# Performance work log

Measured on AMD Instinct MI355X. Metric: run time of the kernel, lower is better.

## Reference

```python
import jax, jax.numpy as jnp
import numpy as np

LN_EPS = 1e-5


def _expert(x, w1, b1, gamma, beta, w2, b2):
    # Linear(input_dim,24) -> LayerNorm(24) -> SiLU -> (Dropout=id in eval) -> Linear(24,16) -> SiLU
    h = x @ w1 + b1                                  # [B,24]
    mu = jnp.mean(h, axis=-1, keepdims=True)
    var = jnp.mean(jnp.square(h - mu), axis=-1, keepdims=True)
    h = (h - mu) * jax.lax.rsqrt(var + LN_EPS) * gamma + beta
    h = jax.nn.silu(h)
    return jax.nn.silu(h @ w2 + b2)                  # [B,16]


def setup_inputs() -> dict:
    key = jax.random.key(0)
    ks = jax.random.split(key, 16)
    D = 16  # input_dim
    s = 0.1
    inp = {
        "x": jax.random.normal(ks[0], (2097152, D), dtype=jnp.float32),
        # gate: Linear(D,8) -> Tanh -> Linear(8,2)
        "gw1": jax.random.normal(ks[1], (D, 8), dtype=jnp.float32) * s,
        "gb1": jnp.zeros((8,), jnp.float32),
        "gw2": jax.random.normal(ks[2], (8, 2), dtype=jnp.float32) * s,
        "gb2": jnp.zeros((2,), jnp.float32),
        # expert1
        "e1w1": jax.random.normal(ks[3], (D, 24), dtype=jnp.float32) * s,
        "e1b1": jnp.zeros((24,), jnp.float32),
        "e1g": jnp.ones((24,), jnp.float32),
        "e1bn": jnp.zeros((24,), jnp.float32),
        "e1w2": jax.random.normal(ks[4], (24, 16), dtype=jnp.float32) * s,
        "e1b2": jnp.zeros((16,), jnp.float32),
        # expert2
        "e2w1": jax.random.normal(ks[5], (D, 24), dtype=jnp.float32) * s,
        "e2b1": jnp.zeros((24,), jnp.float32),
        "e2g": jnp.ones((24,), jnp.float32),
        "e2bn": jnp.zeros((24,), jnp.float32),
        "e2w2": jax.random.normal(ks[6], (24, 16), dtype=jnp.float32) * s,
        "e2b2": jnp.zeros((16,), jnp.float32),
        # trunk: Linear(16,16) -> SiLU -> (Dropout=id)
        "tw": jax.random.normal(ks[7], (16, 16), dtype=jnp.float32) * s,
        "tb": jnp.zeros((16,), jnp.float32),
        # heads
        "sw": jax.random.normal(ks[8], (16, 1), dtype=jnp.float32) * s,
        "sb": jnp.zeros((1,), jnp.float32),
        "hw": jax.random.normal(ks[9], (16, 2), dtype=jnp.float32) * s,
        "hb": jnp.zeros((2,), jnp.float32),
    }
    return inp


def reference(x, gw1, gb1, gw2, gb2,
              e1w1, e1b1, e1g, e1bn, e1w2, e1b2,
              e2w1, e2b1, e2g, e2bn, e2w2, e2b2,
              tw, tb, sw, sb, hw, hb):
    gate_logits = jnp.tanh(x @ gw1 + gb1) @ gw2 + gb2        # [B,2]
    gate_w = jax.nn.softmax(gate_logits, axis=-1)
    h1 = _expert(x, e1w1, e1b1, e1g, e1bn, e1w2, e1b2)       # [B,16]
    h2 = _expert(x, e2w1, e2b1, e2g, e2bn, e2w2, e2b2)       # [B,16]
    h = gate_w[:, :1] * h1 + gate_w[:, 1:] * h2              # [B,16]
    h = jax.nn.silu(h @ tw + tb)                             # trunk (dropout=id)
    strain = h @ sw + sb                                     # [B,1]
    hs = h @ hw + hb                                         # [B,2]
    tensile_raw = hs[:, :1]
    gap = jax.nn.softplus(hs[:, 1:])
    yield_strength = tensile_raw - gap
    return jnp.concatenate([strain, tensile_raw, yield_strength], axis=-1)  # [B,3]
```

## Files before the change

kernel.cpp:

```cpp
#include <hip/hip_runtime.h>

#define LN_EPS 1e-5f

typedef _Float16 f16x4 __attribute__((ext_vector_type(4)));
typedef float f32x4 __attribute__((ext_vector_type(4)));
typedef unsigned int u32;
typedef u32 u32x2 __attribute__((ext_vector_type(2)));

#if defined(__HIP_DEVICE_COMPILE__)
#  if __has_builtin(__builtin_amdgcn_mfma_f32_16x16x16f16)
#    define MFMA16(a, b, c) __builtin_amdgcn_mfma_f32_16x16x16f16(a, b, c, 0, 0, 0)
#  elif __has_builtin(__builtin_amdgcn_mfma_f32_16x16x16_f16)
#    define MFMA16(a, b, c) __builtin_amdgcn_mfma_f32_16x16x16_f16(a, b, c, 0, 0, 0)
#  else
#    error "no 16x16x16 f16 mfma builtin on device"
#  endif
#else
#  define MFMA16(a, b, c) (c)
#endif

__device__ __forceinline__ float fast_rcp(float x) { return __builtin_amdgcn_rcpf(x); }

__device__ __forceinline__ u32 pk2(float a, float b) {
    return __builtin_bit_cast(u32, __builtin_amdgcn_cvt_pkrtz(a, b));
}
__device__ __forceinline__ f16x4 mk4(float a, float b, float c, float d) {
    u32x2 t = {pk2(a, b), pk2(c, d)};
    return __builtin_bit_cast(f16x4, t);
}

__device__ __forceinline__ float silu_f(float a) {
    return a * fast_rcp(1.0f + __expf(-a));
}
__device__ __forceinline__ float tanh_f(float x) {
    return fmaf(2.0f, fast_rcp(1.0f + __expf(-2.0f * x)), -1.0f);
}
__device__ __forceinline__ float softplus_f(float x) {
    float e = __expf(-fabsf(x));
    return fmaxf(x, 0.0f) + __logf(1.0f + e);
}


__device__ __forceinline__ float aval(int m, int row, int k,
                                      const float* gw1, const float* gw2,
                                      const float* e1w1, const float* e1w2,
                                      const float* e2w1, const float* e2w2,
                                      const float* tw, const float* sw, const float* hw) {
    switch (m) {
        case 0:  return (row < 8) ? gw1[k * 8 + row] : 0.0f;
        case 1:  return ((row & 3) < 2 && k < 8) ? gw2[k * 2 + (row & 3)] : 0.0f;
        case 2:  return e1w1[k * 24 + row];
        case 3: {
            if (row < 8) return e1w1[k * 24 + 16 + row];
            if (row == 8) {
                float t = 0.0f;
                for (int j = 0; j < 24; ++j) t += e1w1[k * 24 + j];
                return t * (1.0f / 24.0f);
            }
            return 0.0f;
        }
        case 4:  return e1w2[k * 16 + row];
        case 5:  return (k < 8) ? e1w2[(16 + k) * 16 + row] : 0.0f;
        case 6:  return e2w1[k * 24 + row];
        case 7: {
            if (row < 8) return e2w1[k * 24 + 16 + row];
            if (row == 8) {
                float t = 0.0f;
                for (int j = 0; j < 24; ++j) t += e2w1[k * 24 + j];
                return t * (1.0f / 24.0f);
            }
            return 0.0f;
        }
        case 8:  return e2w2[k * 16 + row];
        case 9:  return (k < 8) ? e2w2[(16 + k) * 16 + row] : 0.0f;
        case 10: return tw[k * 16 + row];
        default:
            if (row == 0) return sw[k];
            if (row == 1) return hw[2 * k + 0];
            if (row == 2) return hw[2 * k + 1];
            return 0.0f;
    }
}

__device__ __forceinline__ float bval(int bf, int row,
                                      const float* gb1, const float* gb2,
                                      const float* e1b1, const float* e1b2,
                                      const float* e2b1, const float* e2b2,
                                      const float* tb, const float* sb, const float* hb) {
    switch (bf) {
        case 0:  return (row < 8) ? gb1[row] : 0.0f;
        case 1:  return ((row & 3) < 2) ? gb2[row & 3] : 0.0f;
        case 2:  return e1b1[row];
        case 3: {
            if (row < 8) return e1b1[16 + row];
            if (row == 8) {
                float t = 0.0f;
                for (int j = 0; j < 24; ++j) t += e1b1[j];
                return t * (1.0f / 24.0f);
            }
            return 0.0f;
        }
        case 4:  return e1b2[row];
        case 5:  return e2b1[row];
        case 6: {
            if (row < 8) return e2b1[16 + row];
            if (row == 8) {
                float t = 0.0f;
                for (int j = 0; j < 24; ++j) t += e2b1[j];
                return t * (1.0f / 24.0f);
            }
            return 0.0f;
        }
        case 7:  return e2b2[row];
        case 8:  return tb[row];
        default:
            if (row == 0) return sb[0];
            if (row == 1) return hb[0];
            if (row == 2) return hb[1];
            return 0.0f;
    }
}

__global__ void pack_frags(const float* __restrict__ gw1, const float* __restrict__ gb1,
                           const float* __restrict__ gw2, const float* __restrict__ gb2,
                           const float* __restrict__ e1w1, const float* __restrict__ e1b1,
                           const float* __restrict__ e1g, const float* __restrict__ e1bn,
                           const float* __restrict__ e1w2, const float* __restrict__ e1b2,
                           const float* __restrict__ e2w1, const float* __restrict__ e2b1,
                           const float* __restrict__ e2g, const float* __restrict__ e2bn,
                           const float* __restrict__ e2w2, const float* __restrict__ e2b2,
                           const float* __restrict__ tw, const float* __restrict__ tb,
                           const float* __restrict__ sw, const float* __restrict__ sb,
                           const float* __restrict__ hw, const float* __restrict__ hb,
                           u32* __restrict__ ws) {
    int t = blockIdx.x * blockDim.x + threadIdx.x;
    if (t < 1536) {
        int m = t >> 7, rem = t & 127, lane = rem >> 1, d = rem & 1;
        int row = lane & 15, k0 = (lane >> 4) * 4 + 2 * d;
        float v0 = aval(m, row, k0,     gw1, gw2, e1w1, e1w2, e2w1, e2w2, tw, sw, hw);
        float v1 = aval(m, row, k0 + 1, gw1, gw2, e1w1, e1w2, e2w1, e2w2, tw, sw, hw);
        ws[t] = pk2(v0, v1);
    } else if (t < 4096) {
        int f = t - 1536;
        int bf = f >> 8, rem = f & 255, lane = rem >> 2, r = rem & 3;
        int row = (lane >> 4) * 4 + r;
        float v = bval(bf, row, gb1, gb2, e1b1, e1b2, e2b1, e2b2, tb, sb, hb);
        ((float*)ws)[t] = v;
    } else if (t < 6144) {
        int f = t - 4096;
        int nf = f >> 8, rem = f & 255, lane = rem >> 2, r = rem & 3;
        int e = nf >> 2, w = nf & 3, g_ = lane >> 4;
        const float* ge = e ? e2g : e1g;
        const float* bne = e ? e2bn : e1bn;
        float v;
        if (w < 2) {
            int feat = g_ * 4 + r;
            v = (w == 0) ? ge[feat] : bne[feat];
        } else {
            int feat = 16 + g_ * 4 + r;
            v = (g_ < 2) ? ((w == 2) ? ge[feat] : bne[feat]) : 0.0f;
        }
        ((float*)ws)[t] = v;
    }
}

__global__ __launch_bounds__(256) void moe_mfma_kernel(const float* __restrict__ x,
                                                       const u32* __restrict__ ws,
                                                       float* __restrict__ out, int nrows) {
    __shared__ u32 lds[6144];
    for (int i = threadIdx.x; i < 6144; i += 256) lds[i] = ws[i];
    __syncthreads();

    int lane = threadIdx.x & 63;
    int g = lane >> 4, s = lane & 15;
    float mask0 = (g == 2) ? 0.0f : 1.0f;
    int wid = (blockIdx.x * blockDim.x + threadIdx.x) >> 6;
    int nw = (gridDim.x * blockDim.x) >> 6;

    auto LA  = [&](int m)  -> f16x4 { return *(const f16x4*)&lds[m * 128 + lane * 2]; };
    auto LB  = [&](int bf) -> f32x4 { return *(const f32x4*)&lds[1536 + bf * 256 + lane * 4]; };
    auto LNF = [&](int nf) -> f32x4 { return *(const f32x4*)&lds[4096 + nf * 256 + lane * 4]; };

    auto expert2 = [&](bool FIRST, int mA1a, int mA1b, int mA2a, int mA2b,
                       int bf1a, int bf1b, int bf2, int nf,
                       f16x4 Bx0, f16x4 Bx1, float sc0, float sc1,
                       f32x4& h0, f32x4& h1) {
        f16x4 A1a = LA(mA1a), A1b = LA(mA1b);
        f32x4 b1a = LB(bf1a), b1b = LB(bf1b);
        f32x4 C1_0 = MFMA16(A1a, Bx0, b1a);
        f32x4 C1_1 = MFMA16(A1a, Bx1, b1a);
        f32x4 C2_0 = MFMA16(A1b, Bx0, b1b);
        f32x4 C2_1 = MFMA16(A1b, Bx1, b1b);

        float mu0 = __shfl(C2_0[0], 32 + s, 64);
        float mu1 = __shfl(C2_1[0], 32 + s, 64);

        float E20 = 0.0f, E21 = 0.0f;
#pragma unroll
        for (int i = 0; i < 4; ++i) {
            E20 = fmaf(C1_0[i], C1_0[i], E20);
            E21 = fmaf(C1_1[i], C1_1[i], E21);
        }
        E20 = fmaf(C2_0[0] * mask0, C2_0[0], E20);
        E21 = fmaf(C2_1[0] * mask0, C2_1[0], E21);
#pragma unroll
        for (int i = 1; i < 4; ++i) {
            E20 = fmaf(C2_0[i], C2_0[i], E20);
            E21 = fmaf(C2_1[i], C2_1[i], E21);
        }
        E20 += __shfl_xor(E20, 16); E20 += __shfl_xor(E20, 32);
        E21 += __shfl_xor(E21, 16); E21 += __shfl_xor(E21, 32);
        float rstd0 = rsqrtf(fmaf(E20, 1.0f / 24.0f, -mu0 * mu0) + LN_EPS);
        float rstd1 = rsqrtf(fmaf(E21, 1.0f / 24.0f, -mu1 * mu1) + LN_EPS);

        f32x4 gc1 = LNF(nf + 0), bc1 = LNF(nf + 1), gc2 = LNF(nf + 2), bc2 = LNF(nf + 3);
        float sv0[8], sv1[8];
#pragma unroll
        for (int i = 0; i < 4; ++i) {
            sv0[i]     = silu_f(fmaf((C1_0[i] - mu0) * rstd0, gc1[i], bc1[i]));
            sv1[i]     = silu_f(fmaf((C1_1[i] - mu1) * rstd1, gc1[i], bc1[i]));
            sv0[4 + i] = silu_f(fmaf((C2_0[i] - mu0) * rstd0, gc2[i], bc2[i]));
            sv1[4 + i] = silu_f(fmaf((C2_1[i] - mu1) * rstd1, gc2[i], bc2[i]));
        }
        f16x4 B1_0 = mk4(sv0[0], sv0[1], sv0[2], sv0[3]);
        f16x4 B2_0 = mk4(sv0[4], sv0[5], sv0[6], sv0[7]);
        f16x4 B1_1 = mk4(sv1[0], sv1[1], sv1[2], sv1[3]);
        f16x4 B2_1 = mk4(sv1[4], sv1[5], sv1[6], sv1[7]);

        f16x4 A2a = LA(mA2a), A2b = LA(mA2b);
        f32x4 b2 = LB(bf2);
        f32x4 O0 = MFMA16(A2a, B1_0, b2);
        f32x4 O1 = MFMA16(A2a, B1_1, b2);
        O0 = MFMA16(A2b, B2_0, O0);
        O1 = MFMA16(A2b, B2_1, O1);

#pragma unroll
        for (int i = 0; i < 4; ++i) {
            float p0 = silu_f(O0[i]);
            float p1 = silu_f(O1[i]);
            if (FIRST) {
                h0[i] = sc0 * p0;
                h1[i] = sc1 * p1;
            } else {
                h0[i] = fmaf(sc0, p0, h0[i]);
                h1[i] = fmaf(sc1, p1, h1[i]);
            }
        }
    };

    int ntiles = (nrows + 15) >> 4;
    int nclamp = nrows - 1;

    auto loadx = [&](int tile) -> f32x4 {
        int r = tile * 16 + s;
        int rc = r < nrows ? r : nclamp;
        return *(const f32x4*)(x + (size_t)rc * 16 + g * 4);
    };

    int p0 = 2 * wid;
    f32x4 xv0, xv1;
    if (p0 < ntiles) {
        xv0 = loadx(p0);
        xv1 = loadx(p0 + 1 < ntiles ? p0 + 1 : p0);
    }

    for (int tp = p0; tp < ntiles; tp += 2 * nw) {
        int tnp = tp + 2 * nw;
        f32x4 xn0, xn1;
        {
            int t0n = tnp < ntiles ? tnp : tp;
            int t1n = tnp + 1 < ntiles ? tnp + 1 : t0n;
            xn0 = loadx(t0n);
            xn1 = loadx(t1n);
        }

        int r0 = tp * 16 + s;
        int r1 = (tp + 1) * 16 + s;
        f16x4 Bx0 = mk4(xv0[0], xv0[1], xv0[2], xv0[3]);
        f16x4 Bx1 = mk4(xv1[0], xv1[1], xv1[2], xv1[3]);

        f32x4 Cg0 = MFMA16(LA(0), Bx0, LB(0));
        f32x4 Cg1 = MFMA16(LA(0), Bx1, LB(0));
        f16x4 Bt0 = mk4(tanh_f(Cg0[0]), tanh_f(Cg0[1]), tanh_f(Cg0[2]), tanh_f(Cg0[3]));
        f16x4 Bt1 = mk4(tanh_f(Cg1[0]), tanh_f(Cg1[1]), tanh_f(Cg1[2]), tanh_f(Cg1[3]));
        f32x4 Cl0 = MFMA16(LA(1), Bt0, LB(1));
        f32x4 Cl1 = MFMA16(LA(1), Bt1, LB(1));
        float w00 = fast_rcp(1.0f + __expf(Cl0[1] - Cl0[0]));
        float w01 = 1.0f - w00;
        float w10 = fast_rcp(1.0f + __expf(Cl1[1] - Cl1[0]));
        float w11 = 1.0f - w10;

        f32x4 h0, h1;
        expert2(true,  2, 3, 4, 5, 2, 3, 4, 0, Bx0, Bx1, w00, w10, h0, h1);
        expert2(false, 6, 7, 8, 9, 5, 6, 7, 4, Bx0, Bx1, w01, w11, h0, h1);

        f16x4 Bh0 = mk4(h0[0], h0[1], h0[2], h0[3]);
        f16x4 Bh1 = mk4(h1[0], h1[1], h1[2], h1[3]);
        f32x4 Ct0 = MFMA16(LA(10), Bh0, LB(8));
        f32x4 Ct1 = MFMA16(LA(10), Bh1, LB(8));
        f16x4 Bu0 = mk4(silu_f(Ct0[0]), silu_f(Ct0[1]), silu_f(Ct0[2]), silu_f(Ct0[3]));
        f16x4 Bu1 = mk4(silu_f(Ct1[0]), silu_f(Ct1[1]), silu_f(Ct1[2]), silu_f(Ct1[3]));

        f32x4 Ch0 = MFMA16(LA(11), Bu0, LB(9));
        f32x4 Ch1 = MFMA16(LA(11), Bu1, LB(9));
        if (g == 0) {
            if (r0 < nrows) {
                float yld = Ch0[1] - softplus_f(Ch0[2]);
                size_t o = (size_t)r0 * 3;
                out[o + 0] = Ch0[0];
                out[o + 1] = Ch0[1];
                out[o + 2] = yld;
            }
            if (r1 < nrows) {
                float yld = Ch1[1] - softplus_f(Ch1[2]);
                size_t o = (size_t)r1 * 3;
                out[o + 0] = Ch1[0];
                out[o + 1] = Ch1[1];
                out[o + 2] = yld;
            }
        }

        xv0 = xn0;
        xv1 = xn1;
    }
}

extern "C" void kernel_launch(void* const* d_in, const int* in_sizes, int n_in,
                              void* d_out, int out_size, void* d_ws, size_t ws_size,
                              hipStream_t stream) {
    const float* x    = (const float*)d_in[0];
    const float* gw1  = (const float*)d_in[1];
    const float* gb1  = (const float*)d_in[2];
    const float* gw2  = (const float*)d_in[3];
    const float* gb2  = (const float*)d_in[4];
    const float* e1w1 = (const float*)d_in[5];
    const float* e1b1 = (const float*)d_in[6];
    const float* e1g  = (const float*)d_in[7];
    const float* e1bn = (const float*)d_in[8];
    const float* e1w2 = (const float*)d_in[9];
    const float* e1b2 = (const float*)d_in[10];
    const float* e2w1 = (const float*)d_in[11];
    const float* e2b1 = (const float*)d_in[12];
    const float* e2g  = (const float*)d_in[13];
    const float* e2bn = (const float*)d_in[14];
    const float* e2w2 = (const float*)d_in[15];
    const float* e2b2 = (const float*)d_in[16];
    const float* tw   = (const float*)d_in[17];
    const float* tb   = (const float*)d_in[18];
    const float* sw   = (const float*)d_in[19];
    const float* sb   = (const float*)d_in[20];
    const float* hw   = (const float*)d_in[21];
    const float* hb   = (const float*)d_in[22];
    float* out = (float*)d_out;
    u32* ws = (u32*)d_ws;

    pack_frags<<<24, 256, 0, stream>>>(gw1, gb1, gw2, gb2,
                                       e1w1, e1b1, e1g, e1bn, e1w2, e1b2,
                                       e2w1, e2b1, e2g, e2bn, e2w2, e2b2,
                                       tw, tb, sw, sb, hw, hb, ws);

    int nrows = in_sizes[0] / 16;
    moe_mfma_kernel<<<2048, 256, 0, stream>>>(x, ws, out, nrows);
}
```

Baseline: 101.6 us.

## Process four row tiles per wave, fold tanh into sigmoid, template out bounds guards

Each wave now handles four 16-row tiles per iteration instead of two, so the LDS fragment loads are amortised and there are more independent MFMA chains to interleave. The gate tanh is rewritten as a sigmoid, with the factor 2 and the -1 offset folded into the packed gate weights and biases. A templated GUARD path drops row clamping and bounds checks when the row count is a multiple of 64. The cost is higher register pressure, and the unguarded prefetch relies on the divisibility check for correctness.

Result: slower. 110.3 us (+8.5%).

```diff
diff --git a/kernel.cpp b/kernel.cpp
--- a/kernel.cpp
+++ b/kernel.cpp
@@ -32,8 +32,8 @@
 __device__ __forceinline__ float silu_f(float a) {
     return a * fast_rcp(1.0f + __expf(-a));
 }
-__device__ __forceinline__ float tanh_f(float x) {
-    return fmaf(2.0f, fast_rcp(1.0f + __expf(-2.0f * x)), -1.0f);
+__device__ __forceinline__ float sig_f(float c) {
+    return fast_rcp(1.0f + __expf(-c));
 }
 __device__ __forceinline__ float softplus_f(float x) {
     float e = __expf(-fabsf(x));
@@ -47,8 +47,8 @@
                                       const float* e2w1, const float* e2w2,
                                       const float* tw, const float* sw, const float* hw) {
     switch (m) {
-        case 0:  return (row < 8) ? gw1[k * 8 + row] : 0.0f;
-        case 1:  return ((row & 3) < 2 && k < 8) ? gw2[k * 2 + (row & 3)] : 0.0f;
+        case 0:  return (row < 8) ? 2.0f * gw1[k * 8 + row] : 0.0f;
+        case 1:  return ((row & 3) < 2 && k < 8) ? 2.0f * gw2[k * 2 + (row & 3)] : 0.0f;
         case 2:  return e1w1[k * 24 + row];
         case 3: {
             if (row < 8) return e1w1[k * 24 + 16 + row];
@@ -83,13 +83,19 @@
 }
 
 __device__ __forceinline__ float bval(int bf, int row,
-                                      const float* gb1, const float* gb2,
+                                      const float* gb1, const float* gb2, const float* gw2,
                                       const float* e1b1, const float* e1b2,
                                       const float* e2b1, const float* e2b2,
                                       const float* tb, const float* sb, const float* hb) {
     switch (bf) {
-        case 0:  return (row < 8) ? gb1[row] : 0.0f;
-        case 1:  return ((row & 3) < 2) ? gb2[row & 3] : 0.0f;
+        case 0:  return (row < 8) ? 2.0f * gb1[row] : 0.0f;
+        case 1: {
+            int j = row & 3;
+            if (j >= 2) return 0.0f;
+            float cs = 0.0f;
+            for (int k = 0; k < 8; ++k) cs += gw2[k * 2 + j];
+            return gb2[j] - cs;
+        }
         case 2:  return e1b1[row];
         case 3: {
             if (row < 8) return e1b1[16 + row];
@@ -144,7 +150,7 @@
         int f = t - 1536;
         int bf = f >> 8, rem = f & 255, lane = rem >> 2, r = rem & 3;
         int row = (lane >> 4) * 4 + r;
-        float v = bval(bf, row, gb1, gb2, e1b1, e1b2, e2b1, e2b2, tb, sb, hb);
+        float v = bval(bf, row, gb1, gb2, gw2, e1b1, e1b2, e2b1, e2b2, tb, sb, hb);
         ((float*)ws)[t] = v;
     } else if (t < 6144) {
         int f = t - 4096;
@@ -164,6 +170,7 @@
     }
 }
 
+template <bool GUARD>
 __global__ __launch_bounds__(256) void moe_mfma_kernel(const float* __restrict__ x,
                                                        const u32* __restrict__ ws,
                                                        float* __restrict__ out, int nrows) {
@@ -181,147 +188,131 @@
     auto LB  = [&](int bf) -> f32x4 { return *(const f32x4*)&lds[1536 + bf * 256 + lane * 4]; };
     auto LNF = [&](int nf) -> f32x4 { return *(const f32x4*)&lds[4096 + nf * 256 + lane * 4]; };
 
-    auto expert2 = [&](bool FIRST, int mA1a, int mA1b, int mA2a, int mA2b,
+    int ntiles = (nrows + 15) >> 4;
+    int nclamp = nrows - 1;
+
+    auto loadx = [&](int tile) -> f32x4 {
+        int r = tile * 16 + s;
+        if (GUARD) r = r < nrows ? r : nclamp;
+        return *(const f32x4*)(x + (size_t)r * 16 + g * 4);
+    };
+
+    auto expert4 = [&](bool FIRST, int mA1a, int mA1b, int mA2a, int mA2b,
                        int bf1a, int bf1b, int bf2, int nf,
-                       f16x4 Bx0, f16x4 Bx1, float sc0, float sc1,
-                       f32x4& h0, f32x4& h1) {
+                       const f16x4 Bx[4], const float sc[4], f32x4 h[4]) {
         f16x4 A1a = LA(mA1a), A1b = LA(mA1b);
         f32x4 b1a = LB(bf1a), b1b = LB(bf1b);
-        f32x4 C1_0 = MFMA16(A1a, Bx0, b1a);
-        f32x4 C1_1 = MFMA16(A1a, Bx1, b1a);
-        f32x4 C2_0 = MFMA16(A1b, Bx0, b1b);
-        f32x4 C2_1 = MFMA16(A1b, Bx1, b1b);
-
-        float mu0 = __shfl(C2_0[0], 32 + s, 64);
-        float mu1 = __shfl(C2_1[0], 32 + s, 64);
-
-        float E20 = 0.0f, E21 = 0.0f;
-#pragma unroll
-        for (int i = 0; i < 4; ++i) {
-            E20 = fmaf(C1_0[i], C1_0[i], E20);
-            E21 = fmaf(C1_1[i], C1_1[i], E21);
-        }
-        E20 = fmaf(C2_0[0] * mask0, C2_0[0], E20);
-        E21 = fmaf(C2_1[0] * mask0, C2_1[0], E21);
-#pragma unroll
-        for (int i = 1; i < 4; ++i) {
-            E20 = fmaf(C2_0[i], C2_0[i], E20);
-            E21 = fmaf(C2_1[i], C2_1[i], E21);
-        }
-        E20 += __shfl_xor(E20, 16); E20 += __shfl_xor(E20, 32);
-        E21 += __shfl_xor(E21, 16); E21 += __shfl_xor(E21, 32);
-        float rstd0 = rsqrtf(fmaf(E20, 1.0f / 24.0f, -mu0 * mu0) + LN_EPS);
-        float rstd1 = rsqrtf(fmaf(E21, 1.0f / 24.0f, -mu1 * mu1) + LN_EPS);
-
+        f32x4 C1[4], C2[4];
+#pragma unroll
+        for (int t = 0; t < 4; ++t) {
+            C1[t] = MFMA16(A1a, Bx[t], b1a);
+            C2[t] = MFMA16(A1b, Bx[t], b1b);
+        }
+        float mu[4], rstd[4];
+#pragma unroll
+        for (int t = 0; t < 4; ++t) mu[t] = __shfl(C2[t][0], 32 + s, 64);
+#pragma unroll
+        for (int t = 0; t < 4; ++t) {
+            float E2 = 0.0f;
+#pragma unroll
+            for (int i = 0; i < 4; ++i) E2 = fmaf(C1[t][i], C1[t][i], E2);
+            E2 = fmaf(C2[t][0] * mask0, C2[t][0], E2);
+#pragma unroll
+            for (int i = 1; i < 4; ++i) E2 = fmaf(C2[t][i], C2[t][i], E2);
+            E2 += __shfl_xor(E2, 16);
+            E2 += __shfl_xor(E2, 32);
+            rstd[t] = rsqrtf(fmaf(E2, 1.0f / 24.0f, -mu[t] * mu[t]) + LN_EPS);
+        }
         f32x4 gc1 = LNF(nf + 0), bc1 = LNF(nf + 1), gc2 = LNF(nf + 2), bc2 = LNF(nf + 3);
-        float sv0[8], sv1[8];
-#pragma unroll
-        for (int i = 0; i < 4; ++i) {
-            sv0[i]     = silu_f(fmaf((C1_0[i] - mu0) * rstd0, gc1[i], bc1[i]));
-            sv1[i]     = silu_f(fmaf((C1_1[i] - mu1) * rstd1, gc1[i], bc1[i]));
-            sv0[4 + i] = silu_f(fmaf((C2_0[i] - mu0) * rstd0, gc2[i], bc2[i]));
-            sv1[4 + i] = silu_f(fmaf((C2_1[i] - mu1) * rstd1, gc2[i], bc2[i]));
-        }
-        f16x4 B1_0 = mk4(sv0[0], sv0[1], sv0[2], sv0[3]);
-        f16x4 B2_0 = mk4(sv0[4], sv0[5], sv0[6], sv0[7]);
-        f16x4 B1_1 = mk4(sv1[0], sv1[1], sv1[2], sv1[3]);
-        f16x4 B2_1 = mk4(sv1[4], sv1[5], sv1[6], sv1[7]);
-
+        f16x4 B1[4], B2[4];
+#pragma unroll
+        for (int t = 0; t < 4; ++t) {
+            float sv[8];
+#pragma unroll
+            for (int i = 0; i < 4; ++i) {
+                sv[i]     = silu_f(fmaf((C1[t][i] - mu[t]) * rstd[t], gc1[i], bc1[i]));
+                sv[4 + i] = silu_f(fmaf((C2[t][i] - mu[t]) * rstd[t], gc2[i], bc2[i]));
+            }
+            B1[t] = mk4(sv[0], sv[1], sv[2], sv[3]);
+            B2[t] = mk4(sv[4], sv[5], sv[6], sv[7]);
+        }
         f16x4 A2a = LA(mA2a), A2b = LA(mA2b);
         f32x4 b2 = LB(bf2);
-        f32x4 O0 = MFMA16(A2a, B1_0, b2);
-        f32x4 O1 = MFMA16(A2a, B1_1, b2);
-        O0 = MFMA16(A2b, B2_0, O0);
-        O1 = MFMA16(A2b, B2_1, O1);
-
-#pragma unroll
-        for (int i = 0; i < 4; ++i) {
-            float p0 = silu_f(O0[i]);
-            float p1 = silu_f(O1[i]);
-            if (FIRST) {
-                h0[i] = sc0 * p0;
-                h1[i] = sc1 * p1;
-            } else {
-                h0[i] = fmaf(sc0, p0, h0[i]);
-                h1[i] = fmaf(sc1, p1, h1[i]);
+#pragma unroll
+        for (int t = 0; t < 4; ++t) {
+            f32x4 O = MFMA16(A2a, B1[t], b2);
+            O = MFMA16(A2b, B2[t], O);
+#pragma unroll
+            for (int i = 0; i < 4; ++i) {
+                float p = silu_f(O[i]);
+                if (FIRST) h[t][i] = sc[t] * p;
+                else       h[t][i] = fmaf(sc[t], p, h[t][i]);
             }
         }
     };
 
-    int ntiles = (nrows + 15) >> 4;
-    int nclamp = nrows - 1;
-
-    auto loadx = [&](int tile) -> f32x4 {
-        int r = tile * 16 + s;
-        int rc = r < nrows ? r : nclamp;
-        return *(const f32x4*)(x + (size_t)rc * 16 + g * 4);
-    };
-
-    int p0 = 2 * wid;
-    f32x4 xv0, xv1;
-    if (p0 < ntiles) {
-        xv0 = loadx(p0);
-        xv1 = loadx(p0 + 1 < ntiles ? p0 + 1 : p0);
-    }
-
-    for (int tp = p0; tp < ntiles; tp += 2 * nw) {
-        int tnp = tp + 2 * nw;
-        f32x4 xn0, xn1;
+    int tq0 = 4 * wid;
+    int stride = 4 * nw;
+    f32x4 xv[4];
+    if (tq0 < ntiles) {
+#pragma unroll
+        for (int t = 0; t < 4; ++t) {
+            int tt = tq0 + t;
+            if (GUARD && tt >= ntiles) tt = ntiles - 1;
+            xv[t] = loadx(tt);
+        }
+    }
+
+    for (int tq = tq0; tq < ntiles; tq += stride) {
+        f32x4 xn[4];
         {
-            int t0n = tnp < ntiles ? tnp : tp;
-            int t1n = tnp + 1 < ntiles ? tnp + 1 : t0n;
-            xn0 = loadx(t0n);
-            xn1 = loadx(t1n);
-        }
-
-        int r0 = tp * 16 + s;
-        int r1 = (tp + 1) * 16 + s;
-        f16x4 Bx0 = mk4(xv0[0], xv0[1], xv0[2], xv0[3]);
-        f16x4 Bx1 = mk4(xv1[0], xv1[1], xv1[2], xv1[3]);
-
-        f32x4 Cg0 = MFMA16(LA(0), Bx0, LB(0));
-        f32x4 Cg1 = MFMA16(LA(0), Bx1, LB(0));
-        f16x4 Bt0 = mk4(tanh_f(Cg0[0]), tanh_f(Cg0[1]), tanh_f(Cg0[2]), tanh_f(Cg0[3]));
-        f16x4 Bt1 = mk4(tanh_f(Cg1[0]), tanh_f(Cg1[1]), tanh_f(Cg1[2]), tanh_f(Cg1[3]));
-        f32x4 Cl0 = MFMA16(LA(1), Bt0, LB(1));
-        f32x4 Cl1 = MFMA16(LA(1), Bt1, LB(1));
-        float w00 = fast_rcp(1.0f + __expf(Cl0[1] - Cl0[0]));
-        float w01 = 1.0f - w00;
-        float w10 = fast_rcp(1.0f + __expf(Cl1[1] - Cl1[0]));
-        float w11 = 1.0f - w10;
-
-        f32x4 h0, h1;
-        expert2(true,  2, 3, 4, 5, 2, 3, 4, 0, Bx0, Bx1, w00, w10, h0, h1);
-        expert2(false, 6, 7, 8, 9, 5, 6, 7, 4, Bx0, Bx1, w01, w11, h0, h1);
-
-        f16x4 Bh0 = mk4(h0[0], h0[1], h0[2], h0[3]);
-        f16x4 Bh1 = mk4(h1[0], h1[1], h1[2], h1[3]);
-        f32x4 Ct0 = MFMA16(LA(10), Bh0, LB(8));
-        f32x4 Ct1 = MFMA16(LA(10), Bh1, LB(8));
-        f16x4 Bu0 = mk4(silu_f(Ct0[0]), silu_f(Ct0[1]), silu_f(Ct0[2]), silu_f(Ct0[3]));
-        f16x4 Bu1 = mk4(silu_f(Ct1[0]), silu_f(Ct1[1]), silu_f(Ct1[2]), silu_f(Ct1[3]));
-
-        f32x4 Ch0 = MFMA16(LA(11), Bu0, LB(9));
-        f32x4 Ch1 = MFMA16(LA(11), Bu1, LB(9));
-        if (g == 0) {
-            if (r0 < nrows) {
-                float yld = Ch0[1] - softplus_f(Ch0[2]);
-                size_t o = (size_t)r0 * 3;
-                out[o + 0] = Ch0[0];
-                out[o + 1] = Ch0[1];
+            int tnq = tq + stride;
+            if (tnq + 3 >= ntiles) tnq = tq;
+#pragma unroll
+            for (int t = 0; t < 4; ++t) xn[t] = loadx(tnq + t);
+        }
+
+        f16x4 Bx[4];
+#pragma unroll
+        for (int t = 0; t < 4; ++t) Bx[t] = mk4(xv[t][0], xv[t][1], xv[t][2], xv[t][3]);
+
+        f16x4 Ag1 = LA(0), Ag2 = LA(1);
+        f32x4 Bg1 = LB(0), Bg2 = LB(1);
+        float w0[4], w1[4];
+#pragma unroll
+        for (int t = 0; t < 4; ++t) {
+            f32x4 Cg = MFMA16(Ag1, Bx[t], Bg1);
+            f16x4 Bt = mk4(sig_f(Cg[0]), sig_f(Cg[1]), sig_f(Cg[2]), sig_f(Cg[3]));
+            f32x4 Cl = MFMA16(Ag2, Bt, Bg2);
+            w0[t] = fast_rcp(1.0f + __expf(Cl[1] - Cl[0]));
+            w1[t] = 1.0f - w0[t];
+        }
+
+        f32x4 h[4];
+        expert4(true,  2, 3, 4, 5, 2, 3, 4, 0, Bx, w0, h);
+        expert4(false, 6, 7, 8, 9, 5, 6, 7, 4, Bx, w1, h);
+
+        f16x4 Atr = LA(10), Ahd = LA(11);
+        f32x4 Btr = LB(8), Bhd = LB(9);
+#pragma unroll
+        for (int t = 0; t < 4; ++t) {
+            f16x4 Bh = mk4(h[t][0], h[t][1], h[t][2], h[t][3]);
+            f32x4 Ct = MFMA16(Atr, Bh, Btr);
+            f16x4 Bu = mk4(silu_f(Ct[0]), silu_f(Ct[1]), silu_f(Ct[2]), silu_f(Ct[3]));
+            f32x4 Ch = MFMA16(Ahd, Bu, Bhd);
+            int r = (tq + t) * 16 + s;
+            bool ok = GUARD ? (g == 0 && r < nrows) : (g == 0);
+            if (ok) {
+                float yld = Ch[1] - softplus_f(Ch[2]);
+                size_t o = (size_t)r * 3;
+                out[o + 0] = Ch[0];
+                out[o + 1] = Ch[1];
                 out[o + 2] = yld;
             }
-            if (r1 < nrows) {
-                float yld = Ch1[1] - softplus_f(Ch1[2]);
-                size_t o = (size_t)r1 * 3;
-                out[o + 0] = Ch1[0];
-                out[o + 1] = Ch1[1];
-                out[o + 2] = yld;
-            }
-        }
-
-        xv0 = xn0;
-        xv1 = xn1;
+        }
+
+#pragma unroll
+        for (int t = 0; t < 4; ++t) xv[t] = xn[t];
     }
 }
 
@@ -360,5 +351,9 @@
                                        tw, tb, sw, sb, hw, hb, ws);
 
     int nrows = in_sizes[0] / 16;
-    moe_mfma_kernel<<<2048, 256, 0, stream>>>(x, ws, out, nrows);
-}
+    if (nrows % 64 == 0) {
+        moe_mfma_kernel<false><<<2048, 256, 0, stream>>>(x, ws, out, nrows);
+    } else {
+        moe_mfma_kernel<true><<<2048, 256, 0, stream>>>(x, ws, out, nrows);
+    }
+}
```
